# Performance work log

Measured on AMD Instinct MI355X. Metric: run time of the kernel, lower is better.

The kernel has to match this reference:

```python
import jax, jax.numpy as jnp
import numpy as np

EPS = 1e-8

def setup_inputs() -> dict:
    key = jax.random.key(0)
    k1, k2 = jax.random.split(key)
    B, IN, OUT, G = 32768, 256, 256, 5
    x = jax.random.normal(k1, (B, IN), dtype=jnp.float32)
    grid = jnp.linspace(-1.0, 1.0, G).astype(jnp.float32)
    coef = jax.random.normal(k2, (OUT, IN, G), dtype=jnp.float32) * 0.1
    scale = jnp.ones((OUT, IN), dtype=jnp.float32)
    bias = jnp.zeros((OUT,), dtype=jnp.float32)
    return {"x": x, "grid": grid, "coef": coef, "scale": scale, "bias": bias}

def reference(x, grid, coef, scale, bias):
    # global min-max normalization to [-1, 1]
    xmin, xmax = x.min(), x.max()
    xn = 2.0 * (x - xmin) / (xmax - xmin + EPS) - 1.0
    # cubic bump B-spline-like basis: (batch, in, grid)
    dist = jnp.abs(xn[..., None] - grid)
    basis = jnp.where(dist < 1.0, 1.0 - dist ** 3, 0.0)
    basis = basis / (basis.sum(axis=-1, keepdims=True) + EPS)
    # fused contraction over (in, grid); equals ((basis*coef).sum(-1)*scale).sum(-1)
    w = coef * scale[..., None]          # (out, in, grid)
    out = jnp.einsum('big,oig->bo', basis, w) + bias
    return out
```

## Files before the change

### kernel.cpp

```cpp
#include <hip/hip_runtime.h>
#include <stdint.h>


#define B_SZ   32768
#define IN_SZ  256
#define OUT_SZ 256
#define KPAD   2048
#define EPSF   1e-8f

#define A_STRIDE 40
#define A_ROWS   64
#define AB_BUF   (A_ROWS * A_STRIDE)
#define BB_BUF   (128 * 32)

typedef __bf16 bf16x8 __attribute__((ext_vector_type(8)));
typedef unsigned short ushort8 __attribute__((ext_vector_type(8)));
typedef float floatx16 __attribute__((ext_vector_type(16)));

__device__ __forceinline__ unsigned short f2bf(float f) {
  unsigned u = __float_as_uint(f);
  u += 0x7FFFu + ((u >> 16) & 1u);
  return (unsigned short)(u >> 16);
}

__global__ void __launch_bounds__(256) wprep_kernel(const float* __restrict__ coef,
                                                    const float* __restrict__ scale,
                                                    unsigned short* __restrict__ w) {
  int idx = blockIdx.x * 256 + threadIdx.x;
  float s = scale[idx];
  const float* c = coef + idx * 5;
  ushort8 v;
  v[0] = f2bf(c[0] * s); v[1] = f2bf(c[1] * s); v[2] = f2bf(c[2] * s);
  v[3] = f2bf(c[3] * s); v[4] = f2bf(c[4] * s);
  v[5] = 0; v[6] = 0; v[7] = 0;
  *(ushort8*)(w + idx * 8) = v;
}

__global__ void __launch_bounds__(256) mm1_kernel(const float* __restrict__ x,
                                                  float* __restrict__ part, int n4) {
  const float4* x4 = (const float4*)x;
  float lmin = 1e30f, lmax = -1e30f;
  for (int i = blockIdx.x * 256 + threadIdx.x; i < n4; i += gridDim.x * 256) {
    float4 v = x4[i];
    lmin = fminf(lmin, fminf(fminf(v.x, v.y), fminf(v.z, v.w)));
    lmax = fmaxf(lmax, fmaxf(fmaxf(v.x, v.y), fmaxf(v.z, v.w)));
  }
  #pragma unroll
  for (int off = 32; off >= 1; off >>= 1) {
    lmin = fminf(lmin, __shfl_down(lmin, off, 64));
    lmax = fmaxf(lmax, __shfl_down(lmax, off, 64));
  }
  __shared__ float smn[4], smx[4];
  int t = threadIdx.x;
  if ((t & 63) == 0) { smn[t >> 6] = lmin; smx[t >> 6] = lmax; }
  __syncthreads();
  if (t == 0) {
    float mn = fminf(fminf(smn[0], smn[1]), fminf(smn[2], smn[3]));
    float mx = fmaxf(fmaxf(smx[0], smx[1]), fmaxf(smx[2], smx[3]));
    part[2 * blockIdx.x] = mn;
    part[2 * blockIdx.x + 1] = mx;
  }
}

__global__ void __launch_bounds__(256) mm2_kernel(const float* __restrict__ part,
                                                  float* __restrict__ scv) {
  int t = threadIdx.x;
  float mn = part[2 * t], mx = part[2 * t + 1];
  #pragma unroll
  for (int off = 32; off >= 1; off >>= 1) {
    mn = fminf(mn, __shfl_down(mn, off, 64));
    mx = fmaxf(mx, __shfl_down(mx, off, 64));
  }
  __shared__ float smn[4], smx[4];
  if ((t & 63) == 0) { smn[t >> 6] = mn; smx[t >> 6] = mx; }
  __syncthreads();
  if (t == 0) {
    mn = fminf(fminf(smn[0], smn[1]), fminf(smn[2], smn[3]));
    mx = fmaxf(fmaxf(smx[0], smx[1]), fmaxf(smx[2], smx[3]));
    float sc = 2.0f / (mx - mn + EPSF);
    scv[0] = sc;
    scv[1] = -mn * sc - 1.0f;
  }
}

__global__ void __launch_bounds__(256, 4) kan_gemm(
    const float* __restrict__ x,
    const unsigned short* __restrict__ w,
    const float* __restrict__ bias,
    const float* __restrict__ scv,
    float* __restrict__ out)
{
  __shared__ __align__(16) unsigned short Ab[2 * AB_BUF];
  __shared__ __align__(16) unsigned short Bb[2 * BB_BUF];

  const int t = threadIdx.x;
  const int lane = t & 63;
  const int wv = t >> 6;
  const int wm = wv & 1, wn = wv >> 1;
  const int l31 = lane & 31, lh = lane >> 5;
  const int bRow = blockIdx.x * 64;
  const int bCol = blockIdx.y * 128;

  const float scA = scv[0];
  const float scB = scv[1];

  const int arow = t >> 2;
  const int slot = t & 3;
  const float* xrow = x + (size_t)(bRow + arow) * IN_SZ;
  unsigned short* awp = Ab + arow * A_STRIDE + slot * 8;

  auto stageB = [&](int kt, int buf) {
    #pragma unroll
    for (int r = 0; r < 2; ++r) {
      int S = r * 256 + t;
      int o = S >> 2, s = S & 3;
      int c4 = (s - (o >> 1)) & 3;
      const unsigned short* g = w + (size_t)(bCol + o) * KPAD + kt * 32 + c4 * 8;
      __builtin_amdgcn_global_load_lds(
          (const __attribute__((address_space(1))) unsigned int*)g,
          (__attribute__((address_space(3))) unsigned int*)(Bb + buf * BB_BUF + S * 8),
          16, 0, 0);
    }
  };

  auto basis = [&](float xval, int buf) {
    float xn = fmaf(xval, scA, scB);
    float d0 = xn + 1.0f, d1 = xn + 0.5f, d2 = xn, d3 = xn - 0.5f, d4 = xn - 1.0f;
    float b0 = fmaxf(fmaf(d0 * d0, -fabsf(d0), 1.0f), 0.0f);
    float b1 = fmaxf(fmaf(d1 * d1, -fabsf(d1), 1.0f), 0.0f);
    float b2 = fmaxf(fmaf(d2 * d2, -fabsf(d2), 1.0f), 0.0f);
    float b3 = fmaxf(fmaf(d3 * d3, -fabsf(d3), 1.0f), 0.0f);
    float b4 = fmaxf(fmaf(d4 * d4, -fabsf(d4), 1.0f), 0.0f);
    float sum = ((b0 + b1) + (b2 + b3)) + (b4 + EPSF);
    float inv = __builtin_amdgcn_rcpf(sum);
    bf16x8 av = {};
    av[0] = (__bf16)(b0 * inv); av[1] = (__bf16)(b1 * inv);
    av[2] = (__bf16)(b2 * inv); av[3] = (__bf16)(b3 * inv);
    av[4] = (__bf16)(b4 * inv);
    *(bf16x8*)(awp + buf * AB_BUF) = av;
  };

  float xvc[8], xvn[8];
  auto loadx = [&](float* xv, int ic) {
    #pragma unroll
    for (int kk = 0; kk < 8; ++kk)
      xv[kk] = xrow[ic * 32 + kk * 4 + slot];
  };

  floatx16 acc[2] = {};

  stageB(0, 0);
  loadx(xvc, 0);
  basis(xvc[0], 0);

  for (int ic = 0; ic < 8; ++ic) {
    #pragma unroll
    for (int kk = 0; kk < 8; ++kk) {
      const int kt = ic * 8 + kk;
      const int cur = kk & 1;
      const int nxt = cur ^ 1;

      __syncthreads();

      if (kt < 63) {
        stageB(kt + 1, nxt);
        if (kk == 1 && ic < 7) loadx(xvn, ic + 1);
        float xp = (kk == 7) ? xvn[0] : xvc[kk + 1];
        basis(xp, nxt);
      }

      #pragma unroll
      for (int ks = 0; ks < 2; ++ks) {
        bf16x8 af = *(const bf16x8*)(Ab + cur * AB_BUF +
                      (wm * 32 + l31) * A_STRIDE + (ks * 2 + lh) * 8);
        #pragma unroll
        for (int ni = 0; ni < 2; ++ni) {
          int o = wn * 64 + ni * 32 + l31;
          int s = ((ks * 2 + lh) + (o >> 1)) & 3;
          bf16x8 bfr = *(const bf16x8*)(Bb + cur * BB_BUF + o * 32 + s * 8);
          acc[ni] = __builtin_amdgcn_mfma_f32_32x32x16_bf16(af, bfr, acc[ni], 0, 0, 0);
        }
      }
    }
    if (ic < 7) {
      #pragma unroll
      for (int kk = 0; kk < 8; ++kk) xvc[kk] = xvn[kk];
    }
  }

  #pragma unroll
  for (int ni = 0; ni < 2; ++ni) {
    int o = bCol + wn * 64 + ni * 32 + l31;
    float bs = bias[o];
    int rb = bRow + wm * 32 + 4 * lh;
    #pragma unroll
    for (int reg = 0; reg < 16; ++reg) {
      int row = rb + (reg & 3) + 8 * (reg >> 2);
      out[(size_t)row * OUT_SZ + o] = acc[ni][reg] + bs;
    }
  }
}

extern "C" void kernel_launch(void* const* d_in, const int* in_sizes, int n_in,
                              void* d_out, int out_size, void* d_ws, size_t ws_size,
                              hipStream_t stream) {
  const float* x     = (const float*)d_in[0];
  const float* coef  = (const float*)d_in[2];
  const float* scale = (const float*)d_in[3];
  const float* bias  = (const float*)d_in[4];
  float* out = (float*)d_out;

  size_t need = 4096 + (size_t)OUT_SZ * KPAD * 2;
  if (ws_size < need) return;

  float* part = (float*)d_ws;
  float* scv  = (float*)((char*)d_ws + 2048);
  unsigned short* w = (unsigned short*)((char*)d_ws + 4096);

  wprep_kernel<<<(OUT_SZ * IN_SZ) / 256, 256, 0, stream>>>(coef, scale, w);
  mm1_kernel<<<256, 256, 0, stream>>>(x, part, (B_SZ * IN_SZ) / 4);
  mm2_kernel<<<1, 256, 0, stream>>>(part, scv);
  dim3 g(B_SZ / 64, OUT_SZ / 128);
  kan_gemm<<<g, 256, 0, stream>>>(x, w, bias, scv, out);
}
```

Measured before the change: 147.7 us.

## Merge prep kernels, load B fragments from global into registers, enlarge M tile

The weight-prep and min/max partial-reduction kernels become one launch. The final min/max reduction moves into the GEMM prologue, which removes two launches. Weights are written in an MFMA-fragment-ordered layout so each wave loads its B fragments straight from global into registers with double buffering, dropping the LDS staging of B. The block tile grows from 64 to 128 rows, with 2x2 accumulators per wave. This doubles B reuse at the cost of more registers and lower occupancy.

```diff
diff --git a/kernel.cpp b/kernel.cpp
--- a/kernel.cpp
+++ b/kernel.cpp
@@ -5,13 +5,10 @@
 #define B_SZ   32768
 #define IN_SZ  256
 #define OUT_SZ 256
-#define KPAD   2048
 #define EPSF   1e-8f
 
 #define A_STRIDE 40
-#define A_ROWS   64
-#define AB_BUF   (A_ROWS * A_STRIDE)
-#define BB_BUF   (128 * 32)
+#define AB_BUF   (128 * A_STRIDE)
 
 typedef __bf16 bf16x8 __attribute__((ext_vector_type(8)));
 typedef unsigned short ushort8 __attribute__((ext_vector_type(8)));
@@ -23,168 +20,161 @@
   return (unsigned short)(u >> 16);
 }
 
-__global__ void __launch_bounds__(256) wprep_kernel(const float* __restrict__ coef,
-                                                    const float* __restrict__ scale,
-                                                    unsigned short* __restrict__ w) {
-  int idx = blockIdx.x * 256 + threadIdx.x;
-  float s = scale[idx];
-  const float* c = coef + idx * 5;
-  ushort8 v;
-  v[0] = f2bf(c[0] * s); v[1] = f2bf(c[1] * s); v[2] = f2bf(c[2] * s);
-  v[3] = f2bf(c[3] * s); v[4] = f2bf(c[4] * s);
-  v[5] = 0; v[6] = 0; v[7] = 0;
-  *(ushort8*)(w + idx * 8) = v;
-}
-
-__global__ void __launch_bounds__(256) mm1_kernel(const float* __restrict__ x,
-                                                  float* __restrict__ part, int n4) {
-  const float4* x4 = (const float4*)x;
-  float lmin = 1e30f, lmax = -1e30f;
-  for (int i = blockIdx.x * 256 + threadIdx.x; i < n4; i += gridDim.x * 256) {
-    float4 v = x4[i];
-    lmin = fminf(lmin, fminf(fminf(v.x, v.y), fminf(v.z, v.w)));
-    lmax = fmaxf(lmax, fmaxf(fmaxf(v.x, v.y), fmaxf(v.z, v.w)));
-  }
-  #pragma unroll
-  for (int off = 32; off >= 1; off >>= 1) {
-    lmin = fminf(lmin, __shfl_down(lmin, off, 64));
-    lmax = fmaxf(lmax, __shfl_down(lmax, off, 64));
-  }
-  __shared__ float smn[4], smx[4];
-  int t = threadIdx.x;
-  if ((t & 63) == 0) { smn[t >> 6] = lmin; smx[t >> 6] = lmax; }
-  __syncthreads();
-  if (t == 0) {
-    float mn = fminf(fminf(smn[0], smn[1]), fminf(smn[2], smn[3]));
-    float mx = fmaxf(fmaxf(smx[0], smx[1]), fmaxf(smx[2], smx[3]));
-    part[2 * blockIdx.x] = mn;
-    part[2 * blockIdx.x + 1] = mx;
-  }
-}
-
-__global__ void __launch_bounds__(256) mm2_kernel(const float* __restrict__ part,
-                                                  float* __restrict__ scv) {
-  int t = threadIdx.x;
-  float mn = part[2 * t], mx = part[2 * t + 1];
-  #pragma unroll
-  for (int off = 32; off >= 1; off >>= 1) {
-    mn = fminf(mn, __shfl_down(mn, off, 64));
-    mx = fmaxf(mx, __shfl_down(mx, off, 64));
-  }
-  __shared__ float smn[4], smx[4];
-  if ((t & 63) == 0) { smn[t >> 6] = mn; smx[t >> 6] = mx; }
-  __syncthreads();
-  if (t == 0) {
-    mn = fminf(fminf(smn[0], smn[1]), fminf(smn[2], smn[3]));
-    mx = fmaxf(fmaxf(smx[0], smx[1]), fmaxf(smx[2], smx[3]));
-    float sc = 2.0f / (mx - mn + EPSF);
-    scv[0] = sc;
-    scv[1] = -mn * sc - 1.0f;
-  }
-}
-
-__global__ void __launch_bounds__(256, 4) kan_gemm(
+
+__global__ void __launch_bounds__(256) prep_kernel(const float* __restrict__ coef,
+                                                   const float* __restrict__ scale,
+                                                   const float* __restrict__ x,
+                                                   unsigned short* __restrict__ wf,
+                                                   float* __restrict__ part, int n4) {
+  const int t = threadIdx.x;
+  if (blockIdx.x < 256) {
+    int idx = blockIdx.x * 256 + t;
+    int o = idx >> 8, i = idx & 255;
+    float s = scale[idx];
+    const float* c = coef + (size_t)idx * 5;
+    ushort8 v;
+    v[0] = f2bf(c[0] * s); v[1] = f2bf(c[1] * s); v[2] = f2bf(c[2] * s);
+    v[3] = f2bf(c[3] * s); v[4] = f2bf(c[4] * s);
+    v[5] = 0; v[6] = 0; v[7] = 0;
+    int chunk = (((o >> 5) * 64 + (i >> 2)) * 2 + ((i >> 1) & 1)) * 64
+                + (i & 1) * 32 + (o & 31);
+    *(ushort8*)(wf + (size_t)chunk * 8) = v;
+  } else {
+    int mb = blockIdx.x - 256;
+    const float4* x4 = (const float4*)x;
+    float lmin = 1e30f, lmax = -1e30f;
+    for (int i = mb * 256 + t; i < n4; i += 256 * 256) {
+      float4 v = x4[i];
+      lmin = fminf(lmin, fminf(fminf(v.x, v.y), fminf(v.z, v.w)));
+      lmax = fmaxf(lmax, fmaxf(fmaxf(v.x, v.y), fmaxf(v.z, v.w)));
+    }
+    #pragma unroll
+    for (int off = 32; off >= 1; off >>= 1) {
+      lmin = fminf(lmin, __shfl_down(lmin, off, 64));
+      lmax = fmaxf(lmax, __shfl_down(lmax, off, 64));
+    }
+    __shared__ float smn[4], smx[4];
+    if ((t & 63) == 0) { smn[t >> 6] = lmin; smx[t >> 6] = lmax; }
+    __syncthreads();
+    if (t == 0) {
+      float mn = fminf(fminf(smn[0], smn[1]), fminf(smn[2], smn[3]));
+      float mx = fmaxf(fmaxf(smx[0], smx[1]), fmaxf(smx[2], smx[3]));
+      part[2 * mb] = mn;
+      part[2 * mb + 1] = mx;
+    }
+  }
+}
+
+__global__ void __launch_bounds__(256, 2) kan_gemm(
     const float* __restrict__ x,
-    const unsigned short* __restrict__ w,
+    const unsigned short* __restrict__ wf,
     const float* __restrict__ bias,
-    const float* __restrict__ scv,
+    const float* __restrict__ part,
     float* __restrict__ out)
 {
   __shared__ __align__(16) unsigned short Ab[2 * AB_BUF];
-  __shared__ __align__(16) unsigned short Bb[2 * BB_BUF];
+  __shared__ float2 red[4];
 
   const int t = threadIdx.x;
   const int lane = t & 63;
   const int wv = t >> 6;
   const int wm = wv & 1, wn = wv >> 1;
   const int l31 = lane & 31, lh = lane >> 5;
-  const int bRow = blockIdx.x * 64;
+  const int bRow = blockIdx.x * 128;
   const int bCol = blockIdx.y * 128;
 
-  const float scA = scv[0];
-  const float scB = scv[1];
-
-  const int arow = t >> 2;
-  const int slot = t & 3;
+  const int ogB = blockIdx.y * 4 + wn * 2;
+  const unsigned short* wfl = wf + (size_t)lane * 8;
+  auto loadB = [&](int kt, bf16x8 (*dst)[2]) {
+    #pragma unroll
+    for (int ks = 0; ks < 2; ++ks)
+      #pragma unroll
+      for (int ni = 0; ni < 2; ++ni)
+        dst[ks][ni] = *(const bf16x8*)(wfl +
+            (size_t)((((ogB + ni) * 64 + kt) * 2 + ks)) * 512);
+  };
+
+  const int arow = t >> 1;
+  const int sl2 = (t & 1) * 2;
   const float* xrow = x + (size_t)(bRow + arow) * IN_SZ;
-  unsigned short* awp = Ab + arow * A_STRIDE + slot * 8;
-
-  auto stageB = [&](int kt, int buf) {
-    #pragma unroll
-    for (int r = 0; r < 2; ++r) {
-      int S = r * 256 + t;
-      int o = S >> 2, s = S & 3;
-      int c4 = (s - (o >> 1)) & 3;
-      const unsigned short* g = w + (size_t)(bCol + o) * KPAD + kt * 32 + c4 * 8;
-      __builtin_amdgcn_global_load_lds(
-          (const __attribute__((address_space(1))) unsigned int*)g,
-          (__attribute__((address_space(3))) unsigned int*)(Bb + buf * BB_BUF + S * 8),
-          16, 0, 0);
+  unsigned short* awp = Ab + arow * A_STRIDE + sl2 * 8;
+
+  bf16x8 bReg[2][2][2];
+  loadB(0, bReg[0]);
+  loadB(1, bReg[1]);
+  float2 xv[2];
+  xv[0] = *(const float2*)(xrow + 0 * 4 + sl2);
+  xv[1] = *(const float2*)(xrow + 1 * 4 + sl2);
+
+  float2 p = ((const float2*)part)[t];
+  float mn = p.x, mx = p.y;
+  #pragma unroll
+  for (int off = 32; off >= 1; off >>= 1) {
+    mn = fminf(mn, __shfl_down(mn, off, 64));
+    mx = fmaxf(mx, __shfl_down(mx, off, 64));
+  }
+  if ((lane) == 0) red[wv] = make_float2(mn, mx);
+  __syncthreads();
+  mn = fminf(fminf(red[0].x, red[1].x), fminf(red[2].x, red[3].x));
+  mx = fmaxf(fmaxf(red[0].y, red[1].y), fmaxf(red[2].y, red[3].y));
+  const float scA = 2.0f / (mx - mn + EPSF);
+  const float scB = -mn * scA - 1.0f;
+
+  auto basis = [&](float2 xp, int buf) {
+    #pragma unroll
+    for (int j = 0; j < 2; ++j) {
+      float xn = fmaf(j ? xp.y : xp.x, scA, scB);
+      float d0 = xn + 1.0f, d1 = xn + 0.5f, d3 = xn - 0.5f, d4 = xn - 1.0f;
+      float b0 = fmaxf(fmaf(d0 * d0, -fabsf(d0), 1.0f), 0.0f);
+      float b1 = fmaxf(fmaf(d1 * d1, -fabsf(d1), 1.0f), 0.0f);
+      float b2 = fmaxf(fmaf(xn * xn, -fabsf(xn), 1.0f), 0.0f);
+      float b3 = fmaxf(fmaf(d3 * d3, -fabsf(d3), 1.0f), 0.0f);
+      float b4 = fmaxf(fmaf(d4 * d4, -fabsf(d4), 1.0f), 0.0f);
+      float sum = ((b0 + b1) + (b2 + b3)) + (b4 + EPSF);
+      float inv = __builtin_amdgcn_rcpf(sum);
+      bf16x8 av = {};
+      av[0] = (__bf16)(b0 * inv); av[1] = (__bf16)(b1 * inv);
+      av[2] = (__bf16)(b2 * inv); av[3] = (__bf16)(b3 * inv);
+      av[4] = (__bf16)(b4 * inv);
+      *(bf16x8*)(awp + buf * AB_BUF + j * 8) = av;
     }
   };
 
-  auto basis = [&](float xval, int buf) {
-    float xn = fmaf(xval, scA, scB);
-    float d0 = xn + 1.0f, d1 = xn + 0.5f, d2 = xn, d3 = xn - 0.5f, d4 = xn - 1.0f;
-    float b0 = fmaxf(fmaf(d0 * d0, -fabsf(d0), 1.0f), 0.0f);
-    float b1 = fmaxf(fmaf(d1 * d1, -fabsf(d1), 1.0f), 0.0f);
-    float b2 = fmaxf(fmaf(d2 * d2, -fabsf(d2), 1.0f), 0.0f);
-    float b3 = fmaxf(fmaf(d3 * d3, -fabsf(d3), 1.0f), 0.0f);
-    float b4 = fmaxf(fmaf(d4 * d4, -fabsf(d4), 1.0f), 0.0f);
-    float sum = ((b0 + b1) + (b2 + b3)) + (b4 + EPSF);
-    float inv = __builtin_amdgcn_rcpf(sum);
-    bf16x8 av = {};
-    av[0] = (__bf16)(b0 * inv); av[1] = (__bf16)(b1 * inv);
-    av[2] = (__bf16)(b2 * inv); av[3] = (__bf16)(b3 * inv);
-    av[4] = (__bf16)(b4 * inv);
-    *(bf16x8*)(awp + buf * AB_BUF) = av;
-  };
-
-  float xvc[8], xvn[8];
-  auto loadx = [&](float* xv, int ic) {
-    #pragma unroll
-    for (int kk = 0; kk < 8; ++kk)
-      xv[kk] = xrow[ic * 32 + kk * 4 + slot];
-  };
-
-  floatx16 acc[2] = {};
-
-  stageB(0, 0);
-  loadx(xvc, 0);
-  basis(xvc[0], 0);
-
-  for (int ic = 0; ic < 8; ++ic) {
-    #pragma unroll
-    for (int kk = 0; kk < 8; ++kk) {
-      const int kt = ic * 8 + kk;
-      const int cur = kk & 1;
-      const int nxt = cur ^ 1;
+  basis(xv[0], 0);
+
+  floatx16 acc[2][2] = {};
+
+  for (int base = 0; base < 64; base += 2) {
+    #pragma unroll
+    for (int u = 0; u < 2; ++u) {
+      const int kt = base + u;
+      const int cur = u, nxt = u ^ 1;
 
       __syncthreads();
 
-      if (kt < 63) {
-        stageB(kt + 1, nxt);
-        if (kk == 1 && ic < 7) loadx(xvn, ic + 1);
-        float xp = (kk == 7) ? xvn[0] : xvc[kk + 1];
-        basis(xp, nxt);
+      bf16x8 af[2][2];
+      #pragma unroll
+      for (int ks = 0; ks < 2; ++ks)
+        #pragma unroll
+        for (int mi = 0; mi < 2; ++mi)
+          af[ks][mi] = *(const bf16x8*)(Ab + cur * AB_BUF +
+              (wm * 64 + mi * 32 + l31) * A_STRIDE + (ks * 2 + lh) * 8);
+
+      if (kt < 63) basis(xv[nxt], nxt);
+
+      #pragma unroll
+      for (int ks = 0; ks < 2; ++ks)
+        #pragma unroll
+        for (int mi = 0; mi < 2; ++mi)
+          #pragma unroll
+          for (int ni = 0; ni < 2; ++ni)
+            acc[mi][ni] = __builtin_amdgcn_mfma_f32_32x32x16_bf16(
+                af[ks][mi], bReg[cur][ks][ni], acc[mi][ni], 0, 0, 0);
+
+      if (kt < 62) {
+        loadB(kt + 2, bReg[cur]);
+        xv[cur] = *(const float2*)(xrow + (kt + 2) * 4 + sl2);
       }
-
-      #pragma unroll
-      for (int ks = 0; ks < 2; ++ks) {
-        bf16x8 af = *(const bf16x8*)(Ab + cur * AB_BUF +
-                      (wm * 32 + l31) * A_STRIDE + (ks * 2 + lh) * 8);
-        #pragma unroll
-        for (int ni = 0; ni < 2; ++ni) {
-          int o = wn * 64 + ni * 32 + l31;
-          int s = ((ks * 2 + lh) + (o >> 1)) & 3;
-          bf16x8 bfr = *(const bf16x8*)(Bb + cur * BB_BUF + o * 32 + s * 8);
-          acc[ni] = __builtin_amdgcn_mfma_f32_32x32x16_bf16(af, bfr, acc[ni], 0, 0, 0);
-        }
-      }
-    }
-    if (ic < 7) {
-      #pragma unroll
-      for (int kk = 0; kk < 8; ++kk) xvc[kk] = xvn[kk];
     }
   }
 
@@ -192,11 +182,14 @@
   for (int ni = 0; ni < 2; ++ni) {
     int o = bCol + wn * 64 + ni * 32 + l31;
     float bs = bias[o];
-    int rb = bRow + wm * 32 + 4 * lh;
-    #pragma unroll
-    for (int reg = 0; reg < 16; ++reg) {
-      int row = rb + (reg & 3) + 8 * (reg >> 2);
-      out[(size_t)row * OUT_SZ + o] = acc[ni][reg] + bs;
+    #pragma unroll
+    for (int mi = 0; mi < 2; ++mi) {
+      int rb = bRow + wm * 64 + mi * 32 + 4 * lh;
+      #pragma unroll
+      for (int reg = 0; reg < 16; ++reg) {
+        int row = rb + (reg & 3) + 8 * (reg >> 2);
+        out[(size_t)row * OUT_SZ + o] = acc[mi][ni][reg] + bs;
+      }
     }
   }
 }
@@ -210,16 +203,14 @@
   const float* bias  = (const float*)d_in[4];
   float* out = (float*)d_out;
 
-  size_t need = 4096 + (size_t)OUT_SZ * KPAD * 2;
+  size_t need = 4096 + (size_t)OUT_SZ * IN_SZ * 8 * 2;
   if (ws_size < need) return;
 
   float* part = (float*)d_ws;
-  float* scv  = (float*)((char*)d_ws + 2048);
-  unsigned short* w = (unsigned short*)((char*)d_ws + 4096);
-
-  wprep_kernel<<<(OUT_SZ * IN_SZ) / 256, 256, 0, stream>>>(coef, scale, w);
-  mm1_kernel<<<256, 256, 0, stream>>>(x, part, (B_SZ * IN_SZ) / 4);
-  mm2_kernel<<<1, 256, 0, stream>>>(part, scv);
-  dim3 g(B_SZ / 64, OUT_SZ / 128);
-  kan_gemm<<<g, 256, 0, stream>>>(x, w, bias, scv, out);
-}
+  unsigned short* wf = (unsigned short*)((char*)d_ws + 4096);
+
+  prep_kernel<<<512, 256, 0, stream>>>(coef, scale, x, wf, part,
+                                       (B_SZ * IN_SZ) / 4);
+  dim3 g(B_SZ / 128, OUT_SZ / 128);
+  kan_gemm<<<g, 256, 0, stream>>>(x, wf, bias, part, out);
+}
```

Measured after the change: 142.4 us. 3.6% less time.
